# Kernel tuning notes

Measured on AMD Instinct MI355X. Metric: run time of the kernel, lower is better.

Reference implementation:

```python
import jax, jax.numpy as jnp
import numpy as np

B, S, D = 2, 2048, 1024
H = 16
HD = D // H  # 64
EPS = 1e-5


def setup_inputs() -> dict:
    key = jax.random.key(0)
    ks = jax.random.split(key, 9)
    s = 1.0 / np.sqrt(D)
    return {
        "x": jax.random.normal(ks[0], (B, S, D), jnp.float32),
        "Wq": jax.random.normal(ks[1], (D, D), jnp.float32) * s,
        "bq": jnp.zeros((D,), jnp.float32),
        "Wk": jax.random.normal(ks[2], (D, D), jnp.float32) * s,
        "bk": jnp.zeros((D,), jnp.float32),
        "Wv": jax.random.normal(ks[3], (D, D), jnp.float32) * s,
        "bv": jnp.zeros((D,), jnp.float32),
        "Wp": jax.random.normal(ks[4], (D, D), jnp.float32) * s,
        "bp": jnp.zeros((D,), jnp.float32),
        "gamma": jnp.ones((D,), jnp.float32),
        "beta": jnp.zeros((D,), jnp.float32),
    }


def reference(x, Wq, bq, Wk, bk, Wv, bv, Wp, bp, gamma, beta):
    # QKV projections -> [B, H, S, HD]
    def split_heads(t):
        return t.reshape(B, S, H, HD).transpose(0, 2, 1, 3)

    q = split_heads(x @ Wq + bq)
    k = split_heads(x @ Wk + bk)
    v = split_heads(x @ Wv + bv)

    scores = jnp.einsum('bhqd,bhkd->bhqk', q, k) / np.sqrt(HD).astype(jnp.float32)
    attn = jax.nn.softmax(scores, axis=-1)  # dropout in eval mode = identity
    out = jnp.einsum('bhqk,bhkd->bhqd', attn, v)
    out = out.transpose(0, 2, 1, 3).reshape(B, S, D)
    out = out @ Wp + bp  # dropout identity

    # residual + LayerNorm over last dim
    y = x + out
    mu = jnp.mean(y, axis=-1, keepdims=True)
    var = jnp.mean((y - mu) ** 2, axis=-1, keepdims=True)
    return (y - mu) / jnp.sqrt(var + EPS) * gamma + beta
```

## Files before the change

kernel.cpp:

```cpp
#include <hip/hip_runtime.h>

#define DI __device__ __forceinline__

typedef __bf16 bf16;
typedef __bf16 bf16x8 __attribute__((ext_vector_type(8)));
typedef __bf16 bf16x4 __attribute__((ext_vector_type(4)));
typedef float  f32x4  __attribute__((ext_vector_type(4)));

DI void async_copy16(const void* g, void* s) {
  __builtin_amdgcn_global_load_lds(
      (__attribute__((address_space(1))) unsigned int*)(void*)g,
      (__attribute__((address_space(3))) unsigned int*)s,
      16, 0, 0);
}

DI f32x4 mfma16(bf16x8 a, bf16x8 b, f32x4 c) {
  return __builtin_amdgcn_mfma_f32_16x16x32_bf16(a, b, c, 0, 0, 0);
}


__global__ __launch_bounds__(256) void convert_x(const float* __restrict__ x,
                                                 bf16* __restrict__ xb) {
  int t = blockIdx.x * 256 + threadIdx.x;
  float4 v = ((const float4*)x)[t];
  bf16x4 o;
  o[0] = (bf16)v.x; o[1] = (bf16)v.y; o[2] = (bf16)v.z; o[3] = (bf16)v.w;
  *(bf16x4*)&xb[t * 4] = o;
}

__global__ __launch_bounds__(256) void transpose_w(const float* __restrict__ Wq,
                                                   const float* __restrict__ Wk,
                                                   const float* __restrict__ Wv,
                                                   const float* __restrict__ Wp,
                                                   bf16* __restrict__ Wt) {
  __shared__ float tile[32][33];
  const float* W = (blockIdx.z == 0) ? Wq : (blockIdx.z == 1) ? Wk
                 : (blockIdx.z == 2) ? Wv : Wp;
  int n0 = blockIdx.x * 32, k0 = blockIdx.y * 32;
  int tx = threadIdx.x, ty = threadIdx.y;
#pragma unroll
  for (int i = 0; i < 4; ++i)
    tile[ty + i * 8][tx] = W[(k0 + ty + i * 8) * 1024 + n0 + tx];
  __syncthreads();
#pragma unroll
  for (int i = 0; i < 4; ++i)
    Wt[((int)blockIdx.z * 1024 + n0 + ty + i * 8) * 1024 + k0 + tx] =
        (bf16)tile[tx][ty + i * 8];
}

template <int MODE, int MT, int NT>
__global__ __launch_bounds__(256, 3) void gemm_bt(
    const bf16* __restrict__ A, const bf16* __restrict__ Bt,
    const float* __restrict__ bias0, const float* __restrict__ bias1,
    const float* __restrict__ bias2, bf16* __restrict__ Qo,
    bf16* __restrict__ Ko, bf16* __restrict__ Vo, float* __restrict__ Po) {
  constexpr int MW = MT / 2, NW = NT / 2;
  constexpr int MI = MW / 16, NI = NW / 16;
  const int tid = threadIdx.x;
  const int w = tid >> 6, lane = tid & 63, quad = lane >> 4, m16 = lane & 15;
  const int m0 = blockIdx.x * MT, n0 = blockIdx.y * NT;
  const int mw = (w >> 1) * MW, nw = (w & 1) * NW;
  const int sw = m16 & 7;

  __shared__ __align__(16) bf16 As[MT * 64];
  __shared__ __align__(16) bf16 Bs[NT * 64];

  f32x4 acc[MI][NI];
#pragma unroll
  for (int i = 0; i < MI; ++i)
#pragma unroll
    for (int j = 0; j < NI; ++j)
#pragma unroll
      for (int r = 0; r < 4; ++r) acc[i][j][r] = 0.0f;

  for (int k0 = 0; k0 < 1024; k0 += 64) {
    __syncthreads();
#pragma unroll
    for (int i = 0; i < MT / 32; ++i) {
      int lin = i * 256 + tid;
      int row = lin >> 3, p = lin & 7;
      async_copy16(&A[(m0 + row) * 1024 + k0 + ((p ^ (row & 7)) << 3)],
                   &As[(i * 256 + w * 64) * 8]);
    }
#pragma unroll
    for (int i = 0; i < NT / 32; ++i) {
      int lin = i * 256 + tid;
      int row = lin >> 3, p = lin & 7;
      async_copy16(&Bt[(n0 + row) * 1024 + k0 + ((p ^ (row & 7)) << 3)],
                   &Bs[(i * 256 + w * 64) * 8]);
    }
    __syncthreads();

#pragma unroll
    for (int kk = 0; kk < 2; ++kk) {
      const int pos = ((kk * 4 + quad) ^ sw) << 3;
      bf16x8 af[MI], bg[NI];
#pragma unroll
      for (int i = 0; i < MI; ++i)
        af[i] = *(const bf16x8*)&As[(mw + i * 16 + m16) * 64 + pos];
#pragma unroll
      for (int j = 0; j < NI; ++j)
        bg[j] = *(const bf16x8*)&Bs[(nw + j * 16 + m16) * 64 + pos];
#pragma unroll
      for (int i = 0; i < MI; ++i)
#pragma unroll
        for (int j = 0; j < NI; ++j) acc[i][j] = mfma16(af[i], bg[j], acc[i][j]);
    }
  }

  const float SC = 0.18033688011112042f;
#pragma unroll
  for (int i = 0; i < MI; ++i) {
#pragma unroll
    for (int j = 0; j < NI; ++j) {
      int np = n0 + nw + j * 16 + m16;
      if (MODE == 0) {
        int which = np >> 10, n = np & 1023;
        float bias = (which == 0) ? bias0[n] : (which == 1) ? bias1[n] : bias2[n];
        int h = n >> 6, hd = n & 63;
        if (which == 2) {
          bf16x4 pv;
          int m = m0 + mw + i * 16 + quad * 4;
          int b = m >> 11, s = m & 2047;
#pragma unroll
          for (int r = 0; r < 4; ++r) pv[r] = (bf16)(acc[i][j][r] + bias);
          *(bf16x4*)&Vo[((b * 16 + h) * 64 + hd) * 2048 + s] = pv;
        } else {
#pragma unroll
          for (int r = 0; r < 4; ++r) {
            int m = m0 + mw + i * 16 + quad * 4 + r;
            int b = m >> 11, s = m & 2047;
            float v = acc[i][j][r] + bias;
            if (which == 0)
              Qo[((b * 16 + h) * 2048 + s) * 64 + hd] = (bf16)(v * SC);
            else
              Ko[((b * 16 + h) * 2048 + s) * 64 + hd] = (bf16)v;
          }
        }
      } else {
        float bias = bias0[np];
#pragma unroll
        for (int r = 0; r < 4; ++r) {
          int m = m0 + mw + i * 16 + quad * 4 + r;
          Po[m * 1024 + np] = acc[i][j][r] + bias;
        }
      }
    }
  }
}

__global__ __launch_bounds__(256, 2) void flash_kernel(const bf16* __restrict__ Q,
                                                       const bf16* __restrict__ K,
                                                       const bf16* __restrict__ Vt,
                                                       bf16* __restrict__ attn) {
  const int S = 2048;
  const int tid = threadIdx.x;
  const int w = tid >> 6, lane = tid & 63, quad = lane >> 4, m16 = lane & 15;
  const int bh = blockIdx.x, b = bh >> 4, h = bh & 15;
  const int qb = blockIdx.y * 128;
  const bf16* Qh = Q + bh * S * 64;
  const bf16* Kh = K + bh * S * 64;
  const bf16* Vh = Vt + bh * 64 * S;

  __shared__ __align__(16) bf16 Ks[2][64 * 64];
  __shared__ __align__(16) bf16 Vs[2][64 * 64];
  __shared__ __align__(16) bf16 Ps[4][16 * 72];

  bf16x8 qf[2][2];
#pragma unroll
  for (int mi = 0; mi < 2; ++mi)
#pragma unroll
    for (int kk = 0; kk < 2; ++kk)
      qf[mi][kk] = *(const bf16x8*)&Qh[(qb + w * 32 + mi * 16 + m16) * 64 +
                                       kk * 32 + quad * 8];

  bf16x8 ones;
#pragma unroll
  for (int j = 0; j < 8; ++j) ones[j] = (bf16)1.0f;

  f32x4 o[2][4];
  f32x4 lacc[2];
#pragma unroll
  for (int mi = 0; mi < 2; ++mi) {
#pragma unroll
    for (int dt = 0; dt < 4; ++dt)
#pragma unroll
      for (int r = 0; r < 4; ++r) o[mi][dt][r] = 0.0f;
#pragma unroll
    for (int r = 0; r < 4; ++r) lacc[mi][r] = 0.0f;
  }

  auto stage = [&](int kb, int buf) {
#pragma unroll
    for (int i = 0; i < 2; ++i) {
      int lin = i * 256 + tid;
      int row = lin >> 3, g = lin & 7;
      async_copy16(&Kh[(kb + row) * 64 + ((g ^ (row & 7)) << 3)],
                   &Ks[buf][(i * 256 + w * 64) * 8]);
      async_copy16(&Vh[row * 2048 + kb + ((g ^ (row & 7)) << 3)],
                   &Vs[buf][(i * 256 + w * 64) * 8]);
    }
  };

  stage(0, 0);

  for (int t = 0; t < 32; ++t) {
    const int cur = t & 1;
    if (t < 31) {
      stage((t + 1) * 64, cur ^ 1);
      asm volatile("s_waitcnt vmcnt(4)" ::: "memory");
    } else {
      asm volatile("s_waitcnt vmcnt(0)" ::: "memory");
    }
    asm volatile("s_barrier" ::: "memory");

    bf16x8 kf[4][2], vf[4][2];
#pragma unroll
    for (int nt = 0; nt < 4; ++nt)
#pragma unroll
      for (int kk = 0; kk < 2; ++kk) {
        int row = nt * 16 + m16;
        int pos = (kk * 4 + quad) ^ (row & 7);
        kf[nt][kk] = *(const bf16x8*)&Ks[cur][row * 64 + pos * 8];
        vf[nt][kk] = *(const bf16x8*)&Vs[cur][row * 64 + pos * 8];
      }
    asm volatile("s_waitcnt lgkmcnt(0)" ::: "memory");
    asm volatile("s_barrier" ::: "memory");

    bf16* Pw = &Ps[w][0];
#pragma unroll
    for (int mi = 0; mi < 2; ++mi) {
      f32x4 sacc[4];
#pragma unroll
      for (int nt = 0; nt < 4; ++nt)
#pragma unroll
        for (int r = 0; r < 4; ++r) sacc[nt][r] = 0.0f;
#pragma unroll
      for (int nt = 0; nt < 4; ++nt)
#pragma unroll
        for (int kk = 0; kk < 2; ++kk)
          sacc[nt] = mfma16(kf[nt][kk], qf[mi][kk], sacc[nt]);

#pragma unroll
      for (int nt = 0; nt < 4; ++nt) {
        bf16x4 p4;
#pragma unroll
        for (int r = 0; r < 4; ++r)
          p4[r] = (bf16)__builtin_amdgcn_exp2f(sacc[nt][r]);
        *(bf16x4*)&Pw[m16 * 72 + nt * 16 + quad * 4] = p4;
      }
      asm volatile("s_waitcnt lgkmcnt(0)" ::: "memory");

      bf16x8 pf[2];
#pragma unroll
      for (int kk = 0; kk < 2; ++kk)
        pf[kk] = *(const bf16x8*)&Pw[m16 * 72 + kk * 32 + quad * 8];

#pragma unroll
      for (int kk = 0; kk < 2; ++kk) lacc[mi] = mfma16(pf[kk], ones, lacc[mi]);

#pragma unroll
      for (int dt = 0; dt < 4; ++dt)
#pragma unroll
        for (int kk = 0; kk < 2; ++kk)
          o[mi][dt] = mfma16(pf[kk], vf[dt][kk], o[mi][dt]);
    }
  }

#pragma unroll
  for (int mi = 0; mi < 2; ++mi) {
    f32x4 inv;
#pragma unroll
    for (int r = 0; r < 4; ++r) inv[r] = 1.0f / lacc[mi][r];
#pragma unroll
    for (int dt = 0; dt < 4; ++dt)
#pragma unroll
      for (int r = 0; r < 4; ++r) {
        int s = qb + w * 32 + mi * 16 + quad * 4 + r;
        int col = h * 64 + dt * 16 + m16;
        attn[(b * 2048 + s) * 1024 + col] = (bf16)(o[mi][dt][r] * inv[r]);
      }
  }
}

__global__ __launch_bounds__(256) void ln_kernel(const float* __restrict__ x,
                                                 const float* __restrict__ pj,
                                                 const float* __restrict__ gamma,
                                                 const float* __restrict__ beta,
                                                 float* __restrict__ out) {
  int row = blockIdx.x, t = threadIdx.x;
  int base = row * 1024 + t * 4;
  float4 xv = *(const float4*)&x[base];
  float4 pv = *(const float4*)&pj[base];
  float y0 = xv.x + pv.x, y1 = xv.y + pv.y, y2 = xv.z + pv.z, y3 = xv.w + pv.w;
  float s = y0 + y1 + y2 + y3;
  float ss = y0 * y0 + y1 * y1 + y2 * y2 + y3 * y3;
  for (int m = 1; m < 64; m <<= 1) {
    s += __shfl_xor(s, m);
    ss += __shfl_xor(ss, m);
  }
  __shared__ float sred[8];
  int w = t >> 6;
  if ((t & 63) == 0) { sred[w * 2] = s; sred[w * 2 + 1] = ss; }
  __syncthreads();
  s = sred[0] + sred[2] + sred[4] + sred[6];
  ss = sred[1] + sred[3] + sred[5] + sred[7];
  float mean = s * (1.0f / 1024.0f);
  float var = ss * (1.0f / 1024.0f) - mean * mean;
  float rstd = rsqrtf(var + 1e-5f);
  float4 gv = *(const float4*)&gamma[t * 4];
  float4 bv = *(const float4*)&beta[t * 4];
  float4 ov;
  ov.x = (y0 - mean) * rstd * gv.x + bv.x;
  ov.y = (y1 - mean) * rstd * gv.y + bv.y;
  ov.z = (y2 - mean) * rstd * gv.z + bv.z;
  ov.w = (y3 - mean) * rstd * gv.w + bv.w;
  *(float4*)&out[base] = ov;
}


extern "C" void kernel_launch(void* const* d_in, const int* in_sizes, int n_in,
                              void* d_out, int out_size, void* d_ws, size_t ws_size,
                              hipStream_t stream) {
  const float* x = (const float*)d_in[0];
  const float* Wq = (const float*)d_in[1];
  const float* bq = (const float*)d_in[2];
  const float* Wk = (const float*)d_in[3];
  const float* bk = (const float*)d_in[4];
  const float* Wv = (const float*)d_in[5];
  const float* bv = (const float*)d_in[6];
  const float* Wp = (const float*)d_in[7];
  const float* bp = (const float*)d_in[8];
  const float* gamma = (const float*)d_in[9];
  const float* beta = (const float*)d_in[10];
  float* out = (float*)d_out;

  char* ws = (char*)d_ws;
  bf16* xb = (bf16*)(ws);
  bf16* Wtb = (bf16*)(ws + (8u << 20));
  bf16* Qb = (bf16*)(ws + (16u << 20));
  bf16* Kb = (bf16*)(ws + (24u << 20));
  bf16* Vtb = (bf16*)(ws + (32u << 20));
  float* proj = (float*)(ws + (16u << 20));
  bf16* attn = xb;

  convert_x<<<4096, 256, 0, stream>>>(x, xb);
  transpose_w<<<dim3(32, 32, 4), dim3(32, 8), 0, stream>>>(Wq, Wk, Wv, Wp, Wtb);
  gemm_bt<0, 128, 128><<<dim3(32, 24), 256, 0, stream>>>(
      xb, Wtb, bq, bk, bv, Qb, Kb, Vtb, nullptr);
  flash_kernel<<<dim3(32, 16), 256, 0, stream>>>(Qb, Kb, Vtb, attn);
  gemm_bt<1, 64, 128><<<dim3(64, 8), 256, 0, stream>>>(
      attn, Wtb + 3072 * 1024, bp, nullptr, nullptr, nullptr, nullptr, nullptr,
      proj);
  ln_kernel<<<4096, 256, 0, stream>>>(x, proj, gamma, beta, out);
}
```

Measured before the change: 189.9 us.

## Merge x conversion into weight transpose launch and batch flash P staging

Folds the x fp32-to-bf16 conversion kernel into the weight transpose kernel as an extra grid slice, which saves one kernel launch. In the flash kernel, both row-tiles' QK^T scores are now computed up front and their exponentials are staged into separate per-warp LDS buffers. A single LDS wait then covers both before the PV MFMAs run. The aim is to cut launch overhead and LDS wait serialization, at the cost of more registers and LDS in the attention kernel.

```diff
diff --git a/kernel.cpp b/kernel.cpp
--- a/kernel.cpp
+++ b/kernel.cpp
@@ -18,26 +18,30 @@
   return __builtin_amdgcn_mfma_f32_16x16x32_bf16(a, b, c, 0, 0, 0);
 }
 
-
-__global__ __launch_bounds__(256) void convert_x(const float* __restrict__ x,
-                                                 bf16* __restrict__ xb) {
-  int t = blockIdx.x * 256 + threadIdx.x;
-  float4 v = ((const float4*)x)[t];
-  bf16x4 o;
-  o[0] = (bf16)v.x; o[1] = (bf16)v.y; o[2] = (bf16)v.z; o[3] = (bf16)v.w;
-  *(bf16x4*)&xb[t * 4] = o;
-}
-
-__global__ __launch_bounds__(256) void transpose_w(const float* __restrict__ Wq,
-                                                   const float* __restrict__ Wk,
-                                                   const float* __restrict__ Wv,
-                                                   const float* __restrict__ Wp,
-                                                   bf16* __restrict__ Wt) {
+__global__ __launch_bounds__(256) void prep(const float* __restrict__ x,
+                                            const float* __restrict__ Wq,
+                                            const float* __restrict__ Wk,
+                                            const float* __restrict__ Wv,
+                                            const float* __restrict__ Wp,
+                                            bf16* __restrict__ xb,
+                                            bf16* __restrict__ Wt) {
+  if (blockIdx.z == 4) {
+    int blk = blockIdx.y * 32 + blockIdx.x;
+    int base = blk * 4096 + threadIdx.x * 4;
+#pragma unroll
+    for (int j = 0; j < 4; ++j) {
+      float4 v = *(const float4*)&x[base + j * 1024];
+      bf16x4 o;
+      o[0] = (bf16)v.x; o[1] = (bf16)v.y; o[2] = (bf16)v.z; o[3] = (bf16)v.w;
+      *(bf16x4*)&xb[base + j * 1024] = o;
+    }
+    return;
+  }
   __shared__ float tile[32][33];
   const float* W = (blockIdx.z == 0) ? Wq : (blockIdx.z == 1) ? Wk
                  : (blockIdx.z == 2) ? Wv : Wp;
   int n0 = blockIdx.x * 32, k0 = blockIdx.y * 32;
-  int tx = threadIdx.x, ty = threadIdx.y;
+  int tx = threadIdx.x & 31, ty = threadIdx.x >> 5;
 #pragma unroll
   for (int i = 0; i < 4; ++i)
     tile[ty + i * 8][tx] = W[(k0 + ty + i * 8) * 1024 + n0 + tx];
@@ -164,7 +168,7 @@
 
   __shared__ __align__(16) bf16 Ks[2][64 * 64];
   __shared__ __align__(16) bf16 Vs[2][64 * 64];
-  __shared__ __align__(16) bf16 Ps[4][16 * 72];
+  __shared__ __align__(16) bf16 Ps[4][2][16 * 72];
 
   bf16x8 qf[2][2];
 #pragma unroll
@@ -227,43 +231,51 @@
     asm volatile("s_waitcnt lgkmcnt(0)" ::: "memory");
     asm volatile("s_barrier" ::: "memory");
 
-    bf16* Pw = &Ps[w][0];
+    f32x4 sacc[2][4];
+#pragma unroll
+    for (int mi = 0; mi < 2; ++mi)
+#pragma unroll
+      for (int nt = 0; nt < 4; ++nt)
+#pragma unroll
+        for (int r = 0; r < 4; ++r) sacc[mi][nt][r] = 0.0f;
+#pragma unroll
+    for (int mi = 0; mi < 2; ++mi)
+#pragma unroll
+      for (int nt = 0; nt < 4; ++nt)
+#pragma unroll
+        for (int kk = 0; kk < 2; ++kk)
+          sacc[mi][nt] = mfma16(kf[nt][kk], qf[mi][kk], sacc[mi][nt]);
+
 #pragma unroll
     for (int mi = 0; mi < 2; ++mi) {
-      f32x4 sacc[4];
-#pragma unroll
-      for (int nt = 0; nt < 4; ++nt)
-#pragma unroll
-        for (int r = 0; r < 4; ++r) sacc[nt][r] = 0.0f;
-#pragma unroll
-      for (int nt = 0; nt < 4; ++nt)
-#pragma unroll
-        for (int kk = 0; kk < 2; ++kk)
-          sacc[nt] = mfma16(kf[nt][kk], qf[mi][kk], sacc[nt]);
-
+      bf16* Pw = &Ps[w][mi][0];
 #pragma unroll
       for (int nt = 0; nt < 4; ++nt) {
         bf16x4 p4;
 #pragma unroll
         for (int r = 0; r < 4; ++r)
-          p4[r] = (bf16)__builtin_amdgcn_exp2f(sacc[nt][r]);
+          p4[r] = (bf16)__builtin_amdgcn_exp2f(sacc[mi][nt][r]);
         *(bf16x4*)&Pw[m16 * 72 + nt * 16 + quad * 4] = p4;
       }
-      asm volatile("s_waitcnt lgkmcnt(0)" ::: "memory");
-
-      bf16x8 pf[2];
+    }
+    asm volatile("s_waitcnt lgkmcnt(0)" ::: "memory");
+
+    bf16x8 pf[2][2];
+#pragma unroll
+    for (int mi = 0; mi < 2; ++mi)
 #pragma unroll
       for (int kk = 0; kk < 2; ++kk)
-        pf[kk] = *(const bf16x8*)&Pw[m16 * 72 + kk * 32 + quad * 8];
-
-#pragma unroll
-      for (int kk = 0; kk < 2; ++kk) lacc[mi] = mfma16(pf[kk], ones, lacc[mi]);
-
+        pf[mi][kk] = *(const bf16x8*)&Ps[w][mi][m16 * 72 + kk * 32 + quad * 8];
+#pragma unroll
+    for (int mi = 0; mi < 2; ++mi) {
+#pragma unroll
+      for (int kk = 0; kk < 2; ++kk)
+        lacc[mi] = mfma16(pf[mi][kk], ones, lacc[mi]);
 #pragma unroll
       for (int dt = 0; dt < 4; ++dt)
 #pragma unroll
         for (int kk = 0; kk < 2; ++kk)
-          o[mi][dt] = mfma16(pf[kk], vf[dt][kk], o[mi][dt]);
+          o[mi][dt] = mfma16(pf[mi][kk], vf[dt][kk], o[mi][dt]);
     }
   }
 
@@ -344,8 +356,7 @@
   float* proj = (float*)(ws + (16u << 20));
   bf16* attn = xb;
 
-  convert_x<<<4096, 256, 0, stream>>>(x, xb);
-  transpose_w<<<dim3(32, 32, 4), dim3(32, 8), 0, stream>>>(Wq, Wk, Wv, Wp, Wtb);
+  prep<<<dim3(32, 32, 5), 256, 0, stream>>>(x, Wq, Wk, Wv, Wp, xb, Wtb);
   gemm_bt<0, 128, 128><<<dim3(32, 24), 256, 0, stream>>>(
       xb, Wtb, bq, bk, bv, Qb, Kb, Vtb, nullptr);
   flash_kernel<<<dim3(32, 16), 256, 0, stream>>>(Qb, Kb, Vtb, attn);
```

New measurement: 188.9 us. No clear change (-0.5%).

## Fuse input conversion kernels and use two-wave 128x128 tiles for QKV GEMM

Applied to the files above, without the earlier changes.

Merges the x-to-bf16 conversion and weight transpose into one prep launch, with z==4 blocks handling the x conversion, which removes one kernel launch. The QKV GEMM now runs with 2 waves per block of 128 threads instead of 4. Each wave computes a 64x128 sub-tile, which doubles the accumulators per wave and gives more MFMA work per LDS fragment load. The risk is higher register pressure, fewer waves to hide the global-to-LDS copies, and a lower launch-bounds occupancy hint of 2.

```diff
diff --git a/kernel.cpp b/kernel.cpp
--- a/kernel.cpp
+++ b/kernel.cpp
@@ -18,26 +18,30 @@
   return __builtin_amdgcn_mfma_f32_16x16x32_bf16(a, b, c, 0, 0, 0);
 }
 
-
-__global__ __launch_bounds__(256) void convert_x(const float* __restrict__ x,
-                                                 bf16* __restrict__ xb) {
-  int t = blockIdx.x * 256 + threadIdx.x;
-  float4 v = ((const float4*)x)[t];
-  bf16x4 o;
-  o[0] = (bf16)v.x; o[1] = (bf16)v.y; o[2] = (bf16)v.z; o[3] = (bf16)v.w;
-  *(bf16x4*)&xb[t * 4] = o;
-}
-
-__global__ __launch_bounds__(256) void transpose_w(const float* __restrict__ Wq,
-                                                   const float* __restrict__ Wk,
-                                                   const float* __restrict__ Wv,
-                                                   const float* __restrict__ Wp,
-                                                   bf16* __restrict__ Wt) {
+__global__ __launch_bounds__(256) void prep(const float* __restrict__ x,
+                                            const float* __restrict__ Wq,
+                                            const float* __restrict__ Wk,
+                                            const float* __restrict__ Wv,
+                                            const float* __restrict__ Wp,
+                                            bf16* __restrict__ xb,
+                                            bf16* __restrict__ Wt) {
+  if (blockIdx.z == 4) {
+    int blk = blockIdx.y * 32 + blockIdx.x;
+    int base = blk * 4096 + threadIdx.x * 4;
+#pragma unroll
+    for (int j = 0; j < 4; ++j) {
+      float4 v = *(const float4*)&x[base + j * 1024];
+      bf16x4 o;
+      o[0] = (bf16)v.x; o[1] = (bf16)v.y; o[2] = (bf16)v.z; o[3] = (bf16)v.w;
+      *(bf16x4*)&xb[base + j * 1024] = o;
+    }
+    return;
+  }
   __shared__ float tile[32][33];
   const float* W = (blockIdx.z == 0) ? Wq : (blockIdx.z == 1) ? Wk
                  : (blockIdx.z == 2) ? Wv : Wp;
   int n0 = blockIdx.x * 32, k0 = blockIdx.y * 32;
-  int tx = threadIdx.x, ty = threadIdx.y;
+  int tx = threadIdx.x & 31, ty = threadIdx.x >> 5;
 #pragma unroll
   for (int i = 0; i < 4; ++i)
     tile[ty + i * 8][tx] = W[(k0 + ty + i * 8) * 1024 + n0 + tx];
@@ -48,18 +52,21 @@
         (bf16)tile[tx][ty + i * 8];
 }
 
-template <int MODE, int MT, int NT>
-__global__ __launch_bounds__(256, 3) void gemm_bt(
+template <int MODE, int MT, int NT, int NW4>
+__global__ __launch_bounds__(NW4 * 64, NW4 == 2 ? 2 : 3) void gemm_bt(
     const bf16* __restrict__ A, const bf16* __restrict__ Bt,
     const float* __restrict__ bias0, const float* __restrict__ bias1,
     const float* __restrict__ bias2, bf16* __restrict__ Qo,
     bf16* __restrict__ Ko, bf16* __restrict__ Vo, float* __restrict__ Po) {
-  constexpr int MW = MT / 2, NW = NT / 2;
-  constexpr int MI = MW / 16, NI = NW / 16;
+  constexpr int NTH = NW4 * 64;
+  constexpr int MW = MT / 2;
+  constexpr int NWc = (NW4 == 4) ? NT / 2 : NT;
+  constexpr int MI = MW / 16, NI = NWc / 16;
   const int tid = threadIdx.x;
   const int w = tid >> 6, lane = tid & 63, quad = lane >> 4, m16 = lane & 15;
   const int m0 = blockIdx.x * MT, n0 = blockIdx.y * NT;
-  const int mw = (w >> 1) * MW, nw = (w & 1) * NW;
+  const int mw = (NW4 == 4 ? (w >> 1) : w) * MW;
+  const int nw = (NW4 == 4 ? (w & 1) : 0) * (NT / 2);
   const int sw = m16 & 7;
 
   __shared__ __align__(16) bf16 As[MT * 64];
@@ -76,18 +83,18 @@
   for (int k0 = 0; k0 < 1024; k0 += 64) {
     __syncthreads();
 #pragma unroll
-    for (int i = 0; i < MT / 32; ++i) {
-      int lin = i * 256 + tid;
+    for (int i = 0; i < MT * 8 / NTH; ++i) {
+      int lin = i * NTH + tid;
       int row = lin >> 3, p = lin & 7;
       async_copy16(&A[(m0 + row) * 1024 + k0 + ((p ^ (row & 7)) << 3)],
-                   &As[(i * 256 + w * 64) * 8]);
-    }
-#pragma unroll
-    for (int i = 0; i < NT / 32; ++i) {
-      int lin = i * 256 + tid;
+                   &As[(i * NTH + w * 64) * 8]);
+    }
+#pragma unroll
+    for (int i = 0; i < NT * 8 / NTH; ++i) {
+      int lin = i * NTH + tid;
       int row = lin >> 3, p = lin & 7;
       async_copy16(&Bt[(n0 + row) * 1024 + k0 + ((p ^ (row & 7)) << 3)],
-                   &Bs[(i * 256 + w * 64) * 8]);
+                   &Bs[(i * NTH + w * 64) * 8]);
     }
     __syncthreads();
 
@@ -344,12 +351,11 @@
   float* proj = (float*)(ws + (16u << 20));
   bf16* attn = xb;
 
-  convert_x<<<4096, 256, 0, stream>>>(x, xb);
-  transpose_w<<<dim3(32, 32, 4), dim3(32, 8), 0, stream>>>(Wq, Wk, Wv, Wp, Wtb);
-  gemm_bt<0, 128, 128><<<dim3(32, 24), 256, 0, stream>>>(
+  prep<<<dim3(32, 32, 5), 256, 0, stream>>>(x, Wq, Wk, Wv, Wp, xb, Wtb);
+  gemm_bt<0, 128, 128, 2><<<dim3(32, 24), 128, 0, stream>>>(
       xb, Wtb, bq, bk, bv, Qb, Kb, Vtb, nullptr);
   flash_kernel<<<dim3(32, 16), 256, 0, stream>>>(Qb, Kb, Vtb, attn);
-  gemm_bt<1, 64, 128><<<dim3(64, 8), 256, 0, stream>>>(
+  gemm_bt<1, 64, 128, 4><<<dim3(64, 8), 256, 0, stream>>>(
       attn, Wtb + 3072 * 1024, bp, nullptr, nullptr, nullptr, nullptr, nullptr,
       proj);
   ln_kernel<<<4096, 256, 0, stream>>>(x, proj, gamma, beta, out);
```

Result: no change. 193.7 us (+2.0%).
